# Kernel tuning notes

Measured on AMD Instinct MI355X. Metric: run time of the kernel, lower is better.

## Reference

```python
import jax, jax.numpy as jnp
import numpy as np

LOWRES = 256  # low-res input to coefficient tower
GB = 16       # spatial_bins (grid H=W)
LB = 8        # luma_bins (grid depth)
NIN, NOUT = 3, 3


def _conv_s2(x, w, b):
    # 3x3 stride-2 conv, torch padding=1
    y = jax.lax.conv_general_dilated(x, w, (2, 2), ((1, 1), (1, 1)),
                                     dimension_numbers=('NCHW', 'OIHW', 'NCHW'))
    return y + b[None, :, None, None]


def _pw(x, w, b):
    # 1x1 conv as einsum; w: [O, C]
    return jnp.einsum('bchw,oc->bohw', x, w) + b[None, :, None, None]


def _bilateral_slice(grid, guide, image):
    # grid [B,12,L,GH,GW]; guide [B,H,W] in [0,1]; image [B,NIN,H,W]
    B, C, L, GH, GW = grid.shape
    H, W = guide.shape[1], guide.shape[2]
    cx = (jnp.arange(W, dtype=jnp.float32) + 0.5) * (GW / W) - 0.5
    cy = (jnp.arange(H, dtype=jnp.float32) + 0.5) * (GH / H) - 0.5
    cz = guide * L - 0.5
    x0f = jnp.floor(cx); wx = cx - x0f
    y0f = jnp.floor(cy); wy = cy - y0f
    z0f = jnp.floor(cz); wz = cz - z0f
    x0 = x0f.astype(jnp.int32); y0 = y0f.astype(jnp.int32); z0 = z0f.astype(jnp.int32)
    bidx = jnp.arange(B)[:, None, None]
    acc = jnp.zeros((B, H, W, C), jnp.float32)
    for dz in (0, 1):
        zi = jnp.clip(z0 + dz, 0, L - 1)                     # [B,H,W]
        wzz = wz if dz else (1.0 - wz)
        for dy in (0, 1):
            yi = jnp.clip(y0 + dy, 0, GH - 1)[None, :, None]
            wyy = (wy if dy else (1.0 - wy))[None, :, None]
            for dx in (0, 1):
                xi = jnp.clip(x0 + dx, 0, GW - 1)[None, None, :]
                wxx = (wx if dx else (1.0 - wx))[None, None, :]
                g = grid[bidx, :, zi, yi, xi]                # [B,H,W,C]
                acc = acc + (wzz * wyy * wxx)[..., None] * g
    aff = acc.reshape(B, H, W, NOUT, NIN + 1)
    out = jnp.einsum('bhwci,bihw->bchw', aff[..., :NIN], image) \
        + jnp.transpose(aff[..., NIN], (0, 3, 1, 2))
    return out


def reference(image, val, sw0, sb0, sw1, sb1, sw2, sb2, sw3, sb3, spw, spb,
              lw1, lb1, lw2, lb2, lw3, lb3, cw, cb, fw1, fb1, fw2, fb2,
              gw, gb, ccm_w, ccm_b, shifts, slopes, prw, prb):
    B = image.shape[0]
    low = jax.image.resize(image, (B, NIN, LOWRES, LOWRES), 'bilinear', antialias=False)
    # splat tower: 4 stride-2 3x3 convs + final 1x1 (no relu)
    x = jax.nn.relu(_conv_s2(low, sw0, sb0))
    x = jax.nn.relu(_conv_s2(x, sw1, sb1))
    x = jax.nn.relu(_conv_s2(x, sw2, sb2))
    x = jax.nn.relu(_conv_s2(x, sw3, sb3))           # [B,64,16,16]
    splat = _pw(x, spw, spb) + val                   # + conditioning value
    # local path: three 1x1 convs with relu
    loc = jax.nn.relu(_pw(splat, lw1, lb1))
    loc = jax.nn.relu(_pw(loc, lw2, lb2))
    loc = jax.nn.relu(_pw(loc, lw3, lb3))            # [B,64,16,16]
    # condition path: 1x1 stride-2 conv -> adaptive avgpool(4) -> 2 fc layers
    c = jax.nn.relu(_pw(splat[:, :, ::2, ::2], cw, cb))  # [B,4,8,8]
    c = c.reshape(B, 4, 4, 2, 4, 2).mean(axis=(3, 5))    # [B,4,4,4]
    c = c.reshape(B, 64)
    c = jax.nn.relu(c @ fw1.T + fb1)
    c = jax.nn.relu(c @ fw2.T + fb2)                 # [B,64]
    fused = jax.nn.relu(c[:, :, None, None] + loc)
    coeff = _pw(fused, gw, gb)                       # [B,96,16,16]
    # split into LB chunks of 12 along channels, stack at dim 2
    grid = coeff.reshape(B, LB, NOUT * (NIN + 1), GB, GB).transpose(0, 2, 1, 3, 4)
    # guidemap: ccm -> piecewise-linear curve -> projection -> hardtanh [0,1]
    g = _pw(image, ccm_w, ccm_b)                     # [B,3,H,W]
    g = (slopes * jax.nn.relu(g[..., None] - shifts[None])).sum(-1)
    g = _pw(g, prw, prb)[:, 0]                       # [B,H,W]
    guide = jnp.clip(g, 0.0, 1.0)
    return _bilateral_slice(grid, guide, image)


def setup_inputs() -> dict:
    rng = np.random.default_rng(0)
    def rn(shape, fan_in):
        return jnp.asarray(rng.standard_normal(shape).astype(np.float32) * np.sqrt(2.0 / fan_in))
    B, H, W = 4, 1024, 1024
    d = {}
    d['image'] = jnp.asarray(rng.random((B, 3, H, W), dtype=np.float32))
    d['val'] = jnp.asarray(rng.random((B, 1, 1, 1), dtype=np.float32))
    # splat tower 3->8->16->32->64
    chans = [(3, 8), (8, 16), (16, 32), (32, 64)]
    for i, (ci, co) in enumerate(chans):
        d[f'sw{i}'] = rn((co, ci, 3, 3), ci * 9)
        d[f'sb{i}'] = jnp.zeros((co,), jnp.float32)
    d['spw'] = rn((64, 64), 64); d['spb'] = jnp.zeros((64,), jnp.float32)
    d['lw1'] = rn((128, 64), 64); d['lb1'] = jnp.zeros((128,), jnp.float32)
    d['lw2'] = rn((128, 128), 128); d['lb2'] = jnp.zeros((128,), jnp.float32)
    d['lw3'] = rn((64, 128), 128); d['lb3'] = jnp.zeros((64,), jnp.float32)
    d['cw'] = rn((4, 64), 64); d['cb'] = jnp.zeros((4,), jnp.float32)
    d['fw1'] = rn((64, 64), 64); d['fb1'] = jnp.zeros((64,), jnp.float32)
    d['fw2'] = rn((64, 64), 64); d['fb2'] = jnp.zeros((64,), jnp.float32)
    d['gw'] = rn((96, 64), 64); d['gb'] = jnp.zeros((96,), jnp.float32)
    # guide params (mirrors make_guide_params init)
    d['ccm_w'] = jnp.asarray(np.identity(3, dtype=np.float32)
                             + rng.standard_normal((3, 3)).astype(np.float32) * 1e-4)
    d['ccm_b'] = jnp.zeros((3,), jnp.float32)
    shifts = np.linspace(0, 1, 16, endpoint=False, dtype=np.float32)[None, None, None, :]
    d['shifts'] = jnp.asarray(np.tile(shifts, (3, 1, 1, 1)))
    slopes = np.zeros((1, 3, 1, 1, 16), dtype=np.float32); slopes[..., 0] = 1.0
    d['slopes'] = jnp.asarray(slopes)
    d['prw'] = jnp.ones((1, 3), jnp.float32) / 3.0
    d['prb'] = jnp.zeros((1,), jnp.float32)
    return d
```

## Files before the change

kernel.cpp:

```cpp
#include <hip/hip_runtime.h>

#define BATCH 4
#define HH 1024
#define WW 1024

__global__ __launch_bounds__(256) void ds01_k(const float* __restrict__ img,
                                              const float* __restrict__ w0,
                                              const float* __restrict__ b0,
                                              const float* __restrict__ w1,
                                              const float* __restrict__ b1,
                                              float* __restrict__ out) {
  int blk = blockIdx.x;
  int tx = blk & 15;
  int ty = (blk >> 4) & 15;
  int b = blk >> 8;
  int t = threadIdx.x;

  __shared__ float low[3][19][21];
  __shared__ float x0s[8][9][12];

  int Y0 = ty << 2, X0 = tx << 2;
  int gy0 = 2 * Y0 - 1, gx0 = 2 * X0 - 1;
  int ly0 = 2 * gy0 - 1, lx0 = 2 * gx0 - 1;

  for (int i = t; i < 3 * 19 * 19; i += 256) {
    int c = i / 361;
    int rem = i - c * 361;
    int ly = rem / 19;
    int lx = rem - ly * 19;
    int gy = ly0 + ly, gx = lx0 + lx;
    float v = 0.f;
    if (gy >= 0 && gx >= 0) {
      const float* p = img + (size_t)(b * 3 + c) * HH * WW + (4 * gy + 1) * WW + 4 * gx;
      float4 u0 = *(const float4*)p;
      float4 u1 = *(const float4*)(p + WW);
      v = 0.25f * (u0.y + u0.z + u1.y + u1.z);
    }
    low[c][ly][lx] = v;
  }
  __syncthreads();

  for (int i = t; i < 8 * 81; i += 256) {
    int ch = i / 81;
    int pos = i - ch * 81;
    int py = pos / 9, px = pos - py * 9;
    int gy = gy0 + py, gx = gx0 + px;
    float v = 0.f;
    if (gy >= 0 && gx >= 0) {
      float a = b0[ch];
#pragma unroll
      for (int ci = 0; ci < 3; ++ci)
#pragma unroll
        for (int ky = 0; ky < 3; ++ky)
#pragma unroll
          for (int kx = 0; kx < 3; ++kx)
            a += low[ci][2 * py + ky][2 * px + kx] *
                 w0[ch * 27 + ci * 9 + ky * 3 + kx];
      v = fmaxf(a, 0.f);
    }
    x0s[ch][py][px] = v;
  }
  __syncthreads();

  {
    int oc = t >> 4;
    int pos = t & 15;
    int y = pos >> 2, x = pos & 3;
    float a = b1[oc];
#pragma unroll
    for (int ci = 0; ci < 8; ++ci)
#pragma unroll
      for (int ky = 0; ky < 3; ++ky)
#pragma unroll
        for (int kx = 0; kx < 3; ++kx)
          a += x0s[ci][2 * y + ky][2 * x + kx] *
               w1[(oc * 8 + ci) * 9 + ky * 3 + kx];
    out[(size_t)(b * 16 + oc) * 64 * 64 + (Y0 + y) * 64 + X0 + x] =
        fmaxf(a, 0.f);
  }
}

template <int CI, int CO, int HI, int P>
__global__ __launch_bounds__(256) void conv_tile_k(const float* __restrict__ in,
                                                   const float* __restrict__ wgt,
                                                   const float* __restrict__ bias,
                                                   float* __restrict__ out) {
  const int HO = HI / 2;
  const int NT = HO / P;
  const int HALO = 2 * P + 1;
  const int RS = 2 * P + 4;
  constexpr int NO = (CO * P * P) / 256;
  int blk = blockIdx.x;
  int tx = blk % NT;
  int ty = (blk / NT) % NT;
  int b = blk / (NT * NT);
  int t = threadIdx.x;

  __shared__ float s[CI][HALO][RS];

  int Y0 = ty * P, X0 = tx * P;
  int gy0 = 2 * Y0 - 1, gx0 = 2 * X0 - 1;

  for (int i = t; i < CI * HALO * HALO; i += 256) {
    int c = i / (HALO * HALO);
    int rem = i - c * (HALO * HALO);
    int ly = rem / HALO;
    int lx = rem - ly * HALO;
    int gy = gy0 + ly, gx = gx0 + lx;
    float v = 0.f;
    if (gy >= 0 && gy < HI && gx >= 0 && gx < HI)
      v = in[((size_t)(b * CI + c) * HI + gy) * HI + gx];
    s[c][ly][lx] = v;
  }
  __syncthreads();

  int px = t % (P * P);
  int og = t / (P * P);
  int x = px % P, y = px / P;
  float acc[NO];
#pragma unroll
  for (int j = 0; j < NO; ++j) acc[j] = bias[og * NO + j];
  for (int ci = 0; ci < CI; ++ci) {
#pragma unroll
    for (int ky = 0; ky < 3; ++ky) {
#pragma unroll
      for (int kx = 0; kx < 3; ++kx) {
        float v = s[ci][2 * y + ky][2 * x + kx];
#pragma unroll
        for (int j = 0; j < NO; ++j)
          acc[j] += wgt[((og * NO + j) * CI + ci) * 9 + ky * 3 + kx] * v;
      }
    }
  }
#pragma unroll
  for (int j = 0; j < NO; ++j)
    out[(size_t)(b * CO + og * NO + j) * HO * HO + (Y0 + y) * HO + X0 + x] =
        fmaxf(acc[j], 0.f);
}

template <int CI, int RELU>
__device__ __forceinline__ void pw4_c64(const float (*__restrict__ X)[4],
                                        float (*__restrict__ Y)[4],
                                        const float* __restrict__ w,
                                        const float* __restrict__ bias,
                                        float badd, int t) {
  int u = t & 3, og = t >> 2;
  float acc = bias[og] + badd;
#pragma unroll 4
  for (int k = 0; k < CI; k += 4) {
    float4 wv = *(const float4*)&w[og * CI + k];
    acc += wv.x * X[k][u] + wv.y * X[k + 1][u] + wv.z * X[k + 2][u] +
           wv.w * X[k + 3][u];
  }
  if (RELU) acc = fmaxf(acc, 0.f);
  Y[og][u] = acc;
}

template <int CI, int RELU>
__device__ __forceinline__ void pw4_c128(const float (*__restrict__ X)[4],
                                         float (*__restrict__ Y)[4],
                                         const float* __restrict__ w,
                                         const float* __restrict__ bias,
                                         int t) {
  int u0 = (t & 1) << 1, og = t >> 1;
  float a0 = bias[og], a1 = a0;
#pragma unroll 4
  for (int k = 0; k < CI; k += 4) {
    float4 wv = *(const float4*)&w[og * CI + k];
    float2 x0 = *(const float2*)&X[k][u0];
    float2 x1 = *(const float2*)&X[k + 1][u0];
    float2 x2 = *(const float2*)&X[k + 2][u0];
    float2 x3v = *(const float2*)&X[k + 3][u0];
    a0 += wv.x * x0.x + wv.y * x1.x + wv.z * x2.x + wv.w * x3v.x;
    a1 += wv.x * x0.y + wv.y * x1.y + wv.z * x2.y + wv.w * x3v.y;
  }
  if (RELU) { a0 = fmaxf(a0, 0.f); a1 = fmaxf(a1, 0.f); }
  Y[og][u0] = a0;
  Y[og][u0 + 1] = a1;
}

__global__ __launch_bounds__(256) void mlp_k(
    const float* __restrict__ x3, const float* __restrict__ spw,
    const float* __restrict__ spb, const float* __restrict__ val,
    const float* __restrict__ lw1, const float* __restrict__ lb1,
    const float* __restrict__ lw2, const float* __restrict__ lb2,
    const float* __restrict__ lw3, const float* __restrict__ lb3,
    const float* __restrict__ cw, const float* __restrict__ cb,
    const float* __restrict__ fw1, const float* __restrict__ fb1,
    const float* __restrict__ fw2, const float* __restrict__ fb2,
    const float* __restrict__ gw, const float* __restrict__ gb,
    float* __restrict__ gridt) {
  int blk = blockIdx.x;
  int b = blk >> 6;
  int p0 = (blk & 63) << 2;
  int t = threadIdx.x;

  __shared__ __align__(16) float A[128][4];
  __shared__ __align__(16) float Bf[128][4];
  __shared__ float effs[4][64];
  __shared__ float ebv[4];
  __shared__ float s8v[4][64];
  __shared__ float scv[64], h1v[64], f2v[64];

  A[t >> 2][t & 3] = x3[((size_t)(b * 64 + (t >> 2))) * 256 + p0 + (t & 3)];
  {
    int ch = t >> 6, k = t & 63;
    float a = 0.f;
#pragma unroll 8
    for (int o = 0; o < 64; ++o) a += cw[ch * 64 + o] * spw[o * 64 + k];
    effs[ch][k] = a;
    if (k == 0) {
      float a2 = 0.f;
      float vb = val[b];
#pragma unroll 8
      for (int o = 0; o < 64; ++o) a2 += cw[ch * 64 + o] * (spb[o] + vb);
      ebv[ch] = cb[ch] + a2;
    }
  }
  __syncthreads();
  {
    int ch = t >> 6, i = t & 63;
    int p = ((i >> 3) << 5) + ((i & 7) << 1);
    float a = ebv[ch];
#pragma unroll 8
    for (int k = 0; k < 64; ++k)
      a += effs[ch][k] * x3[((size_t)(b * 64 + k)) * 256 + p];
    s8v[ch][i] = fmaxf(a, 0.f);
  }
  __syncthreads();
  if (t < 64) {
    int ch = t >> 4, q = t & 15;
    int py = q >> 2, qx = q & 3;
    int i0 = (py * 2) * 8 + qx * 2;
    scv[t] = 0.25f * (s8v[ch][i0] + s8v[ch][i0 + 1] + s8v[ch][i0 + 8] +
                      s8v[ch][i0 + 9]);
  }
  __syncthreads();

  if (t < 64) {
    float a = fb1[t];
#pragma unroll 8
    for (int k = 0; k < 64; ++k) a += fw1[t * 64 + k] * scv[k];
    h1v[t] = fmaxf(a, 0.f);
  }
  pw4_c64<64, 0>(A, Bf, spw, spb, val[b], t);
  __syncthreads();
  if (t < 64) {
    float a = fb2[t];
#pragma unroll 8
    for (int k = 0; k < 64; ++k) a += fw2[t * 64 + k] * h1v[k];
    f2v[t] = fmaxf(a, 0.f);
  }
  pw4_c128<64, 1>(Bf, A, lw1, lb1, t);
  __syncthreads();
  pw4_c128<128, 1>(A, Bf, lw2, lb2, t);
  __syncthreads();
  pw4_c64<128, 1>(Bf, A, lw3, lb3, 0.f, t);
  __syncthreads();

  {
    int u0 = (t & 1) << 1, og = t >> 1;
    if (og < 96) {
      float a0 = gb[og], a1 = a0;
#pragma unroll 4
      for (int k = 0; k < 64; k += 4) {
        float4 cc4 = *(const float4*)&f2v[k];
        float2 x0 = *(const float2*)&A[k][u0];
        float2 x1 = *(const float2*)&A[k + 1][u0];
        float2 x2 = *(const float2*)&A[k + 2][u0];
        float2 x3v = *(const float2*)&A[k + 3][u0];
        x0.x = fmaxf(x0.x + cc4.x, 0.f); x0.y = fmaxf(x0.y + cc4.x, 0.f);
        x1.x = fmaxf(x1.x + cc4.y, 0.f); x1.y = fmaxf(x1.y + cc4.y, 0.f);
        x2.x = fmaxf(x2.x + cc4.z, 0.f); x2.y = fmaxf(x2.y + cc4.z, 0.f);
        x3v.x = fmaxf(x3v.x + cc4.w, 0.f); x3v.y = fmaxf(x3v.y + cc4.w, 0.f);
        float4 wv = *(const float4*)&gw[og * 64 + k];
        a0 += wv.x * x0.x + wv.y * x1.x + wv.z * x2.x + wv.w * x3v.x;
        a1 += wv.x * x0.y + wv.y * x1.y + wv.z * x2.y + wv.w * x3v.y;
      }
      int l = og / 12, cc = og - l * 12;
      gridt[(size_t)(((b * 8 + l) << 8) + p0 + u0) * 12 + cc] = a0;
      gridt[(size_t)(((b * 8 + l) << 8) + p0 + u0 + 1) * 12 + cc] = a1;
    }
  }
}

#define ZST 200
__global__ __launch_bounds__(256, 6) void slice_k(
    const float* __restrict__ img, const float* __restrict__ gridt,
    const float* __restrict__ ccm_w, const float* __restrict__ ccm_b,
    const float* __restrict__ shifts, const float* __restrict__ slopes,
    const float* __restrict__ prw, const float* __restrict__ prb,
    float* __restrict__ out) {
  int blk = blockIdx.x;
  int b = blk >> 10;
  int h = blk & 1023;
  int t = threadIdx.x;

  __shared__ float sg[8 * ZST];
  __shared__ float2 lut[3][16];

  float cy = (h + 0.5f) * 0.015625f - 0.5f;
  float y0f = floorf(cy);
  float wy = cy - y0f;
  int y0 = (int)y0f;
  int yi0 = min(max(y0, 0), 15), yi1 = min(max(y0 + 1, 0), 15);

  if (t < 48) {
    int c = t >> 4, k = t & 15;
    float cs = 0.f, cbv = 0.f;
    for (int i = 0; i <= k; ++i) {
      float s = slopes[c * 16 + i];
      cs += s;
      cbv += s * shifts[c * 16 + i];
    }
    lut[c][k] = make_float2(cs, cbv);
  }

  for (int i = t; i < 384; i += 256) {
    int z = i / 48;
    int e = i - z * 48;
    const float4* s0 =
        (const float4*)(gridt + (size_t)(((b * 8 + z) << 8) + (yi0 << 4)) * 12);
    const float4* s1 =
        (const float4*)(gridt + (size_t)(((b * 8 + z) << 8) + (yi1 << 4)) * 12);
    float4 a = s0[e], c = s1[e];
    float4 v = make_float4(a.x + wy * (c.x - a.x), a.y + wy * (c.y - a.y),
                           a.z + wy * (c.z - a.z), a.w + wy * (c.w - a.w));
    *((float4*)(sg + z * ZST) + e) = v;
  }
  __syncthreads();

  int pp = (h << 10) + (t << 2);
  const float* ib = img + (size_t)b * 3 * HH * WW;
  float4 R4 = *(const float4*)(ib + pp);
  float4 G4 = *(const float4*)(ib + HH * WW + pp);
  float4 B4 = *(const float4*)(ib + 2 * HH * WW + pp);
  float r_[4] = {R4.x, R4.y, R4.z, R4.w};
  float g_[4] = {G4.x, G4.y, G4.z, G4.w};
  float b_[4] = {B4.x, B4.y, B4.z, B4.w};

  float m0 = ccm_w[0], m1 = ccm_w[1], m2 = ccm_w[2];
  float m3 = ccm_w[3], m4 = ccm_w[4], m5 = ccm_w[5];
  float m6 = ccm_w[6], m7 = ccm_w[7], m8 = ccm_w[8];
  float c0 = ccm_b[0], c1 = ccm_b[1], c2 = ccm_b[2];
  float p0 = prw[0], p1 = prw[1], p2 = prw[2], pb = prb[0];

  float base0 = shifts[0], base1 = shifts[16], base2 = shifts[32];
  float inv0 = 1.0f / (shifts[1] - base0);
  float inv1 = 1.0f / (shifts[17] - base1);
  float inv2 = 1.0f / (shifts[33] - base2);

  float ro[4], go[4], bo[4];
#pragma unroll
  for (int j = 0; j < 4; ++j) {
    float r = r_[j], g = g_[j], bl = b_[j];
    float v0 = c0 + m0 * r + m1 * g + m2 * bl;
    float v1 = c1 + m3 * r + m4 * g + m5 * bl;
    float v2 = c2 + m6 * r + m7 * g + m8 * bl;

    float tv0 = fmaxf(v0, base0);
    float tv1 = fmaxf(v1, base1);
    float tv2 = fmaxf(v2, base2);
    int j0 = min((int)((tv0 - base0) * inv0), 15);
    int j1 = min((int)((tv1 - base1) * inv1), 15);
    int j2 = min((int)((tv2 - base2) * inv2), 15);
    float2 e0 = lut[0][j0];
    float2 e1 = lut[1][j1];
    float2 e2 = lut[2][j2];
    float f0 = e0.x * tv0 - e0.y;
    float f1 = e1.x * tv1 - e1.y;
    float f2 = e2.x * tv2 - e2.y;

    float gg = pb + p0 * f0 + p1 * f1 + p2 * f2;
    float guide = fminf(fmaxf(gg, 0.f), 1.f);

    int w = (t << 2) + j;
    float cx = (w + 0.5f) * 0.015625f - 0.5f;
    float x0f = floorf(cx);
    float wx = cx - x0f;
    int x0i = (int)x0f;
    int xi0 = min(max(x0i, 0), 15), xi1 = min(max(x0i + 1, 0), 15);

    float cz = guide * 8.0f - 0.5f;
    float z0f = floorf(cz);
    float wz = cz - z0f;
    int z0i = (int)z0f;
    int zi0 = min(max(z0i, 0), 7), zi1 = min(max(z0i + 1, 0), 7);

    int oz0 = zi0 * ZST, oz1 = zi1 * ZST;
    int ox0 = xi0 * 12, ox1 = xi1 * 12;
    float wz1 = wz, wz0 = 1.f - wz;
    float wx1 = wx, wx0 = 1.f - wx;

    float rr = 0.f, gg2 = 0.f, bb2 = 0.f;
#pragma unroll
    for (int dz = 0; dz < 2; ++dz) {
      int oz = dz ? oz1 : oz0;
      float wzz = dz ? wz1 : wz0;
#pragma unroll
      for (int dx = 0; dx < 2; ++dx) {
        int ox = dx ? ox1 : ox0;
        float wgt = wzz * (dx ? wx1 : wx0);
        const float* gp = sg + oz + ox;
        float4 a0 = *(const float4*)gp;
        float4 a1 = *(const float4*)(gp + 4);
        float4 a2 = *(const float4*)(gp + 8);
        rr  += wgt * (a0.x * r + a0.y * g + a0.z * bl + a0.w);
        gg2 += wgt * (a1.x * r + a1.y * g + a1.z * bl + a1.w);
        bb2 += wgt * (a2.x * r + a2.y * g + a2.z * bl + a2.w);
      }
    }
    ro[j] = rr;
    go[j] = gg2;
    bo[j] = bb2;
  }
  float* ob = out + (size_t)b * 3 * HH * WW;
  *(float4*)(ob + pp) = make_float4(ro[0], ro[1], ro[2], ro[3]);
  *(float4*)(ob + HH * WW + pp) = make_float4(go[0], go[1], go[2], go[3]);
  *(float4*)(ob + 2 * HH * WW + pp) = make_float4(bo[0], bo[1], bo[2], bo[3]);
}

extern "C" void kernel_launch(void* const* d_in, const int* in_sizes, int n_in,
                              void* d_out, int out_size, void* d_ws, size_t ws_size,
                              hipStream_t stream) {
  const float* image = (const float*)d_in[0];
  const float* val   = (const float*)d_in[1];
  const float* sw0 = (const float*)d_in[2];  const float* sb0 = (const float*)d_in[3];
  const float* sw1 = (const float*)d_in[4];  const float* sb1 = (const float*)d_in[5];
  const float* sw2 = (const float*)d_in[6];  const float* sb2 = (const float*)d_in[7];
  const float* sw3 = (const float*)d_in[8];  const float* sb3 = (const float*)d_in[9];
  const float* spw = (const float*)d_in[10]; const float* spb = (const float*)d_in[11];
  const float* lw1 = (const float*)d_in[12]; const float* lb1 = (const float*)d_in[13];
  const float* lw2 = (const float*)d_in[14]; const float* lb2 = (const float*)d_in[15];
  const float* lw3 = (const float*)d_in[16]; const float* lb3 = (const float*)d_in[17];
  const float* cw  = (const float*)d_in[18]; const float* cb  = (const float*)d_in[19];
  const float* fw1 = (const float*)d_in[20]; const float* fb1 = (const float*)d_in[21];
  const float* fw2 = (const float*)d_in[22]; const float* fb2 = (const float*)d_in[23];
  const float* gw  = (const float*)d_in[24]; const float* gb  = (const float*)d_in[25];
  const float* ccm_w = (const float*)d_in[26]; const float* ccm_b = (const float*)d_in[27];
  const float* shifts = (const float*)d_in[28]; const float* slopes = (const float*)d_in[29];
  const float* prw = (const float*)d_in[30]; const float* prb = (const float*)d_in[31];
  float* out = (float*)d_out;

  float* ws    = (float*)d_ws;
  float* x0    = ws;
  float* x1    = x0 + 524288;
  float* x2    = x1 + 262144;
  float* x3    = x2 + 131072;
  float* gridt = x3 + 65536 + 256;

  ds01_k<<<1024, 256, 0, stream>>>(image, sw0, sb0, sw1, sb1, x1);
  conv_tile_k<16, 32, 64, 4><<<256, 256, 0, stream>>>(x1, sw2, sb2, x2);
  conv_tile_k<32, 64, 32, 2><<<256, 256, 0, stream>>>(x2, sw3, sb3, x3);
  mlp_k<<<256, 256, 0, stream>>>(x3, spw, spb, val, lw1, lb1, lw2, lb2, lw3, lb3,
                                 cw, cb, fw1, fb1, fw2, fb2, gw, gb, gridt);
  slice_k<<<4096, 256, 0, stream>>>(image, gridt, ccm_w, ccm_b, shifts, slopes,
                                    prw, prb, out);
}
```

Measured before the change: 223.1 us.

## Fuse conv2, conv3 and MLP into one persistent kernel with grid barriers

Merges the two strided conv kernels and the MLP/grid kernel into a single 256-block kernel that separates stages with atomic-counter grid barriers. The counters are reset inside ds01_k. The aim is to remove two kernel launch gaps on tiny stages. The risks are barrier spin cost, and a deadlock if all 256 blocks are not co-resident, though the MI355X has enough CUs for this.

```diff
diff --git a/kernel.cpp b/kernel.cpp
--- a/kernel.cpp
+++ b/kernel.cpp
@@ -3,18 +3,32 @@
 #define BATCH 4
 #define HH 1024
 #define WW 1024
+
+__device__ __forceinline__ void gbar(unsigned* cnt) {
+  __syncthreads();
+  __threadfence();
+  if (threadIdx.x == 0) {
+    atomicAdd(cnt, 1u);
+    while (atomicAdd(cnt, 0u) < 256u) __builtin_amdgcn_s_sleep(2);
+  }
+  __syncthreads();
+  __threadfence();
+}
 
 __global__ __launch_bounds__(256) void ds01_k(const float* __restrict__ img,
                                               const float* __restrict__ w0,
                                               const float* __restrict__ b0,
                                               const float* __restrict__ w1,
                                               const float* __restrict__ b1,
-                                              float* __restrict__ out) {
+                                              float* __restrict__ out,
+                                              unsigned* __restrict__ cnt) {
   int blk = blockIdx.x;
   int tx = blk & 15;
   int ty = (blk >> 4) & 15;
   int b = blk >> 8;
   int t = threadIdx.x;
+
+  if (blk == 0 && t < 2) cnt[t] = 0;
 
   __shared__ float low[3][19][21];
   __shared__ float x0s[8][9][12];
@@ -80,108 +94,14 @@
   }
 }
 
-template <int CI, int CO, int HI, int P>
-__global__ __launch_bounds__(256) void conv_tile_k(const float* __restrict__ in,
-                                                   const float* __restrict__ wgt,
-                                                   const float* __restrict__ bias,
-                                                   float* __restrict__ out) {
-  const int HO = HI / 2;
-  const int NT = HO / P;
-  const int HALO = 2 * P + 1;
-  const int RS = 2 * P + 4;
-  constexpr int NO = (CO * P * P) / 256;
-  int blk = blockIdx.x;
-  int tx = blk % NT;
-  int ty = (blk / NT) % NT;
-  int b = blk / (NT * NT);
-  int t = threadIdx.x;
-
-  __shared__ float s[CI][HALO][RS];
-
-  int Y0 = ty * P, X0 = tx * P;
-  int gy0 = 2 * Y0 - 1, gx0 = 2 * X0 - 1;
-
-  for (int i = t; i < CI * HALO * HALO; i += 256) {
-    int c = i / (HALO * HALO);
-    int rem = i - c * (HALO * HALO);
-    int ly = rem / HALO;
-    int lx = rem - ly * HALO;
-    int gy = gy0 + ly, gx = gx0 + lx;
-    float v = 0.f;
-    if (gy >= 0 && gy < HI && gx >= 0 && gx < HI)
-      v = in[((size_t)(b * CI + c) * HI + gy) * HI + gx];
-    s[c][ly][lx] = v;
-  }
-  __syncthreads();
-
-  int px = t % (P * P);
-  int og = t / (P * P);
-  int x = px % P, y = px / P;
-  float acc[NO];
-#pragma unroll
-  for (int j = 0; j < NO; ++j) acc[j] = bias[og * NO + j];
-  for (int ci = 0; ci < CI; ++ci) {
-#pragma unroll
-    for (int ky = 0; ky < 3; ++ky) {
-#pragma unroll
-      for (int kx = 0; kx < 3; ++kx) {
-        float v = s[ci][2 * y + ky][2 * x + kx];
-#pragma unroll
-        for (int j = 0; j < NO; ++j)
-          acc[j] += wgt[((og * NO + j) * CI + ci) * 9 + ky * 3 + kx] * v;
-      }
-    }
-  }
-#pragma unroll
-  for (int j = 0; j < NO; ++j)
-    out[(size_t)(b * CO + og * NO + j) * HO * HO + (Y0 + y) * HO + X0 + x] =
-        fmaxf(acc[j], 0.f);
-}
-
-template <int CI, int RELU>
-__device__ __forceinline__ void pw4_c64(const float (*__restrict__ X)[4],
-                                        float (*__restrict__ Y)[4],
-                                        const float* __restrict__ w,
-                                        const float* __restrict__ bias,
-                                        float badd, int t) {
-  int u = t & 3, og = t >> 2;
-  float acc = bias[og] + badd;
-#pragma unroll 4
-  for (int k = 0; k < CI; k += 4) {
-    float4 wv = *(const float4*)&w[og * CI + k];
-    acc += wv.x * X[k][u] + wv.y * X[k + 1][u] + wv.z * X[k + 2][u] +
-           wv.w * X[k + 3][u];
-  }
-  if (RELU) acc = fmaxf(acc, 0.f);
-  Y[og][u] = acc;
-}
-
-template <int CI, int RELU>
-__device__ __forceinline__ void pw4_c128(const float (*__restrict__ X)[4],
-                                         float (*__restrict__ Y)[4],
-                                         const float* __restrict__ w,
-                                         const float* __restrict__ bias,
-                                         int t) {
-  int u0 = (t & 1) << 1, og = t >> 1;
-  float a0 = bias[og], a1 = a0;
-#pragma unroll 4
-  for (int k = 0; k < CI; k += 4) {
-    float4 wv = *(const float4*)&w[og * CI + k];
-    float2 x0 = *(const float2*)&X[k][u0];
-    float2 x1 = *(const float2*)&X[k + 1][u0];
-    float2 x2 = *(const float2*)&X[k + 2][u0];
-    float2 x3v = *(const float2*)&X[k + 3][u0];
-    a0 += wv.x * x0.x + wv.y * x1.x + wv.z * x2.x + wv.w * x3v.x;
-    a1 += wv.x * x0.y + wv.y * x1.y + wv.z * x2.y + wv.w * x3v.y;
-  }
-  if (RELU) { a0 = fmaxf(a0, 0.f); a1 = fmaxf(a1, 0.f); }
-  Y[og][u0] = a0;
-  Y[og][u0 + 1] = a1;
-}
-
-__global__ __launch_bounds__(256) void mlp_k(
-    const float* __restrict__ x3, const float* __restrict__ spw,
-    const float* __restrict__ spb, const float* __restrict__ val,
+__global__ __launch_bounds__(256, 1) void mid_k(
+    const float* __restrict__ x1,
+    const float* __restrict__ sw2, const float* __restrict__ sb2,
+    float* __restrict__ x2,
+    const float* __restrict__ sw3, const float* __restrict__ sb3,
+    float* __restrict__ x3,
+    const float* __restrict__ spw, const float* __restrict__ spb,
+    const float* __restrict__ val,
     const float* __restrict__ lw1, const float* __restrict__ lb1,
     const float* __restrict__ lw2, const float* __restrict__ lb2,
     const float* __restrict__ lw3, const float* __restrict__ lb3,
@@ -189,12 +109,12 @@
     const float* __restrict__ fw1, const float* __restrict__ fb1,
     const float* __restrict__ fw2, const float* __restrict__ fb2,
     const float* __restrict__ gw, const float* __restrict__ gb,
-    float* __restrict__ gridt) {
+    float* __restrict__ gridt, unsigned* __restrict__ cnt) {
   int blk = blockIdx.x;
-  int b = blk >> 6;
-  int p0 = (blk & 63) << 2;
   int t = threadIdx.x;
 
+  __shared__ float s2[16][9][12];
+  __shared__ float s3[32][5][8];
   __shared__ __align__(16) float A[128][4];
   __shared__ __align__(16) float Bf[128][4];
   __shared__ float effs[4][64];
@@ -202,84 +122,201 @@
   __shared__ float s8v[4][64];
   __shared__ float scv[64], h1v[64], f2v[64];
 
-  A[t >> 2][t & 3] = x3[((size_t)(b * 64 + (t >> 2))) * 256 + p0 + (t & 3)];
   {
-    int ch = t >> 6, k = t & 63;
-    float a = 0.f;
+    int tx = blk & 7, ty = (blk >> 3) & 7, b = blk >> 6;
+    int Y0 = ty * 4, X0 = tx * 4;
+    int gy0 = 2 * Y0 - 1, gx0 = 2 * X0 - 1;
+    for (int i = t; i < 16 * 81; i += 256) {
+      int c = i / 81;
+      int rem = i - c * 81;
+      int ly = rem / 9, lx = rem - ly * 9;
+      int gy = gy0 + ly, gx = gx0 + lx;
+      float v = 0.f;
+      if (gy >= 0 && gy < 64 && gx >= 0 && gx < 64)
+        v = x1[((size_t)(b * 16 + c) * 64 + gy) * 64 + gx];
+      s2[c][ly][lx] = v;
+    }
+    __syncthreads();
+    int px = t & 15, og = t >> 4;
+    int x = px & 3, y = px >> 2;
+    float a0 = sb2[og * 2], a1 = sb2[og * 2 + 1];
+    for (int ci = 0; ci < 16; ++ci) {
+#pragma unroll
+      for (int ky = 0; ky < 3; ++ky)
+#pragma unroll
+        for (int kx = 0; kx < 3; ++kx) {
+          float v = s2[ci][2 * y + ky][2 * x + kx];
+          a0 += sw2[((og * 2) * 16 + ci) * 9 + ky * 3 + kx] * v;
+          a1 += sw2[((og * 2 + 1) * 16 + ci) * 9 + ky * 3 + kx] * v;
+        }
+    }
+    x2[(size_t)(b * 32 + og * 2) * 1024 + (Y0 + y) * 32 + X0 + x] = fmaxf(a0, 0.f);
+    x2[(size_t)(b * 32 + og * 2 + 1) * 1024 + (Y0 + y) * 32 + X0 + x] = fmaxf(a1, 0.f);
+  }
+  gbar(cnt + 0);
+
+  {
+    int tx = blk & 7, ty = (blk >> 3) & 7, b = blk >> 6;
+    int Y0 = ty * 2, X0 = tx * 2;
+    int gy0 = 2 * Y0 - 1, gx0 = 2 * X0 - 1;
+    for (int i = t; i < 32 * 25; i += 256) {
+      int c = i / 25;
+      int rem = i - c * 25;
+      int ly = rem / 5, lx = rem - ly * 5;
+      int gy = gy0 + ly, gx = gx0 + lx;
+      float v = 0.f;
+      if (gy >= 0 && gy < 32 && gx >= 0 && gx < 32)
+        v = x2[((size_t)(b * 32 + c) * 32 + gy) * 32 + gx];
+      s3[c][ly][lx] = v;
+    }
+    __syncthreads();
+    int px = t & 3, og = t >> 2;
+    int x = px & 1, y = px >> 1;
+    float a = sb3[og];
+    for (int ci = 0; ci < 32; ++ci) {
+#pragma unroll
+      for (int ky = 0; ky < 3; ++ky)
+#pragma unroll
+        for (int kx = 0; kx < 3; ++kx)
+          a += sw3[(og * 32 + ci) * 9 + ky * 3 + kx] *
+               s3[ci][2 * y + ky][2 * x + kx];
+    }
+    x3[(size_t)(b * 64 + og) * 256 + (Y0 + y) * 16 + X0 + x] = fmaxf(a, 0.f);
+  }
+  gbar(cnt + 1);
+
+  {
+    int b = blk >> 6;
+    int p0 = (blk & 63) << 2;
+
+    A[t >> 2][t & 3] = x3[((size_t)(b * 64 + (t >> 2))) * 256 + p0 + (t & 3)];
+    {
+      int ch = t >> 6, k = t & 63;
+      float a = 0.f;
 #pragma unroll 8
-    for (int o = 0; o < 64; ++o) a += cw[ch * 64 + o] * spw[o * 64 + k];
-    effs[ch][k] = a;
-    if (k == 0) {
-      float a2 = 0.f;
-      float vb = val[b];
+      for (int o = 0; o < 64; ++o) a += cw[ch * 64 + o] * spw[o * 64 + k];
+      effs[ch][k] = a;
+      if (k == 0) {
+        float a2 = 0.f;
+        float vb = val[b];
 #pragma unroll 8
-      for (int o = 0; o < 64; ++o) a2 += cw[ch * 64 + o] * (spb[o] + vb);
-      ebv[ch] = cb[ch] + a2;
-    }
-  }
-  __syncthreads();
-  {
-    int ch = t >> 6, i = t & 63;
-    int p = ((i >> 3) << 5) + ((i & 7) << 1);
-    float a = ebv[ch];
+        for (int o = 0; o < 64; ++o) a2 += cw[ch * 64 + o] * (spb[o] + vb);
+        ebv[ch] = cb[ch] + a2;
+      }
+    }
+    __syncthreads();
+    {
+      int ch = t >> 6, i = t & 63;
+      int p = ((i >> 3) << 5) + ((i & 7) << 1);
+      float a = ebv[ch];
 #pragma unroll 8
-    for (int k = 0; k < 64; ++k)
-      a += effs[ch][k] * x3[((size_t)(b * 64 + k)) * 256 + p];
-    s8v[ch][i] = fmaxf(a, 0.f);
-  }
-  __syncthreads();
-  if (t < 64) {
-    int ch = t >> 4, q = t & 15;
-    int py = q >> 2, qx = q & 3;
-    int i0 = (py * 2) * 8 + qx * 2;
-    scv[t] = 0.25f * (s8v[ch][i0] + s8v[ch][i0 + 1] + s8v[ch][i0 + 8] +
-                      s8v[ch][i0 + 9]);
-  }
-  __syncthreads();
-
-  if (t < 64) {
-    float a = fb1[t];
+      for (int k = 0; k < 64; ++k)
+        a += effs[ch][k] * x3[((size_t)(b * 64 + k)) * 256 + p];
+      s8v[ch][i] = fmaxf(a, 0.f);
+    }
+    __syncthreads();
+    if (t < 64) {
+      int ch = t >> 4, q = t & 15;
+      int py = q >> 2, qx = q & 3;
+      int i0 = (py * 2) * 8 + qx * 2;
+      scv[t] = 0.25f * (s8v[ch][i0] + s8v[ch][i0 + 1] + s8v[ch][i0 + 8] +
+                        s8v[ch][i0 + 9]);
+    }
+    __syncthreads();
+
+    if (t < 64) {
+      float a = fb1[t];
 #pragma unroll 8
-    for (int k = 0; k < 64; ++k) a += fw1[t * 64 + k] * scv[k];
-    h1v[t] = fmaxf(a, 0.f);
-  }
-  pw4_c64<64, 0>(A, Bf, spw, spb, val[b], t);
-  __syncthreads();
-  if (t < 64) {
-    float a = fb2[t];
-#pragma unroll 8
-    for (int k = 0; k < 64; ++k) a += fw2[t * 64 + k] * h1v[k];
-    f2v[t] = fmaxf(a, 0.f);
-  }
-  pw4_c128<64, 1>(Bf, A, lw1, lb1, t);
-  __syncthreads();
-  pw4_c128<128, 1>(A, Bf, lw2, lb2, t);
-  __syncthreads();
-  pw4_c64<128, 1>(Bf, A, lw3, lb3, 0.f, t);
-  __syncthreads();
-
-  {
-    int u0 = (t & 1) << 1, og = t >> 1;
-    if (og < 96) {
-      float a0 = gb[og], a1 = a0;
+      for (int k = 0; k < 64; ++k) a += fw1[t * 64 + k] * scv[k];
+      h1v[t] = fmaxf(a, 0.f);
+    }
+    {
+      int u = t & 3, og = t >> 2;
+      float acc = spb[og] + val[b];
 #pragma unroll 4
       for (int k = 0; k < 64; k += 4) {
-        float4 cc4 = *(const float4*)&f2v[k];
-        float2 x0 = *(const float2*)&A[k][u0];
-        float2 x1 = *(const float2*)&A[k + 1][u0];
-        float2 x2 = *(const float2*)&A[k + 2][u0];
-        float2 x3v = *(const float2*)&A[k + 3][u0];
-        x0.x = fmaxf(x0.x + cc4.x, 0.f); x0.y = fmaxf(x0.y + cc4.x, 0.f);
-        x1.x = fmaxf(x1.x + cc4.y, 0.f); x1.y = fmaxf(x1.y + cc4.y, 0.f);
-        x2.x = fmaxf(x2.x + cc4.z, 0.f); x2.y = fmaxf(x2.y + cc4.z, 0.f);
-        x3v.x = fmaxf(x3v.x + cc4.w, 0.f); x3v.y = fmaxf(x3v.y + cc4.w, 0.f);
-        float4 wv = *(const float4*)&gw[og * 64 + k];
-        a0 += wv.x * x0.x + wv.y * x1.x + wv.z * x2.x + wv.w * x3v.x;
-        a1 += wv.x * x0.y + wv.y * x1.y + wv.z * x2.y + wv.w * x3v.y;
-      }
-      int l = og / 12, cc = og - l * 12;
-      gridt[(size_t)(((b * 8 + l) << 8) + p0 + u0) * 12 + cc] = a0;
-      gridt[(size_t)(((b * 8 + l) << 8) + p0 + u0 + 1) * 12 + cc] = a1;
+        float4 wv = *(const float4*)&spw[og * 64 + k];
+        acc += wv.x * A[k][u] + wv.y * A[k + 1][u] + wv.z * A[k + 2][u] +
+               wv.w * A[k + 3][u];
+      }
+      Bf[og][u] = acc;
+    }
+    __syncthreads();
+    if (t < 64) {
+      float a = fb2[t];
+#pragma unroll 8
+      for (int k = 0; k < 64; ++k) a += fw2[t * 64 + k] * h1v[k];
+      f2v[t] = fmaxf(a, 0.f);
+    }
+    {
+      int u0 = (t & 1) << 1, og = t >> 1;
+      float a0 = lb1[og], a1 = a0;
+#pragma unroll 4
+      for (int k = 0; k < 64; k += 4) {
+        float4 wv = *(const float4*)&lw1[og * 64 + k];
+        float2 q0 = *(const float2*)&Bf[k][u0];
+        float2 q1 = *(const float2*)&Bf[k + 1][u0];
+        float2 q2 = *(const float2*)&Bf[k + 2][u0];
+        float2 q3 = *(const float2*)&Bf[k + 3][u0];
+        a0 += wv.x * q0.x + wv.y * q1.x + wv.z * q2.x + wv.w * q3.x;
+        a1 += wv.x * q0.y + wv.y * q1.y + wv.z * q2.y + wv.w * q3.y;
+      }
+      A[og][u0] = fmaxf(a0, 0.f);
+      A[og][u0 + 1] = fmaxf(a1, 0.f);
+    }
+    __syncthreads();
+    {
+      int u0 = (t & 1) << 1, og = t >> 1;
+      float a0 = lb2[og], a1 = a0;
+#pragma unroll 4
+      for (int k = 0; k < 128; k += 4) {
+        float4 wv = *(const float4*)&lw2[og * 128 + k];
+        float2 q0 = *(const float2*)&A[k][u0];
+        float2 q1 = *(const float2*)&A[k + 1][u0];
+        float2 q2 = *(const float2*)&A[k + 2][u0];
+        float2 q3 = *(const float2*)&A[k + 3][u0];
+        a0 += wv.x * q0.x + wv.y * q1.x + wv.z * q2.x + wv.w * q3.x;
+        a1 += wv.x * q0.y + wv.y * q1.y + wv.z * q2.y + wv.w * q3.y;
+      }
+      Bf[og][u0] = fmaxf(a0, 0.f);
+      Bf[og][u0 + 1] = fmaxf(a1, 0.f);
+    }
+    __syncthreads();
+    {
+      int u = t & 3, og = t >> 2;
+      float acc = lb3[og];
+#pragma unroll 4
+      for (int k = 0; k < 128; k += 4) {
+        float4 wv = *(const float4*)&lw3[og * 128 + k];
+        acc += wv.x * Bf[k][u] + wv.y * Bf[k + 1][u] + wv.z * Bf[k + 2][u] +
+               wv.w * Bf[k + 3][u];
+      }
+      A[og][u] = fmaxf(acc, 0.f);
+    }
+    __syncthreads();
+    {
+      int u0 = (t & 1) << 1, og = t >> 1;
+      if (og < 96) {
+        float a0 = gb[og], a1 = a0;
+#pragma unroll 4
+        for (int k = 0; k < 64; k += 4) {
+          float4 cc4 = *(const float4*)&f2v[k];
+          float2 q0 = *(const float2*)&A[k][u0];
+          float2 q1 = *(const float2*)&A[k + 1][u0];
+          float2 q2 = *(const float2*)&A[k + 2][u0];
+          float2 q3 = *(const float2*)&A[k + 3][u0];
+          q0.x = fmaxf(q0.x + cc4.x, 0.f); q0.y = fmaxf(q0.y + cc4.x, 0.f);
+          q1.x = fmaxf(q1.x + cc4.y, 0.f); q1.y = fmaxf(q1.y + cc4.y, 0.f);
+          q2.x = fmaxf(q2.x + cc4.z, 0.f); q2.y = fmaxf(q2.y + cc4.z, 0.f);
+          q3.x = fmaxf(q3.x + cc4.w, 0.f); q3.y = fmaxf(q3.y + cc4.w, 0.f);
+          float4 wv = *(const float4*)&gw[og * 64 + k];
+          a0 += wv.x * q0.x + wv.y * q1.x + wv.z * q2.x + wv.w * q3.x;
+          a1 += wv.x * q0.y + wv.y * q1.y + wv.z * q2.y + wv.w * q3.y;
+        }
+        int l = og / 12, cc = og - l * 12;
+        gridt[(size_t)(((b * 8 + l) << 8) + p0 + u0) * 12 + cc] = a0;
+        gridt[(size_t)(((b * 8 + l) << 8) + p0 + u0 + 1) * 12 + cc] = a1;
+      }
     }
   }
 }
@@ -448,12 +485,12 @@
   float* x2    = x1 + 262144;
   float* x3    = x2 + 131072;
   float* gridt = x3 + 65536 + 256;
-
-  ds01_k<<<1024, 256, 0, stream>>>(image, sw0, sb0, sw1, sb1, x1);
-  conv_tile_k<16, 32, 64, 4><<<256, 256, 0, stream>>>(x1, sw2, sb2, x2);
-  conv_tile_k<32, 64, 32, 2><<<256, 256, 0, stream>>>(x2, sw3, sb3, x3);
-  mlp_k<<<256, 256, 0, stream>>>(x3, spw, spb, val, lw1, lb1, lw2, lb2, lw3, lb3,
-                                 cw, cb, fw1, fb1, fw2, fb2, gw, gb, gridt);
+  unsigned* cnt = (unsigned*)(gridt + 98304);
+
+  ds01_k<<<1024, 256, 0, stream>>>(image, sw0, sb0, sw1, sb1, x1, cnt);
+  mid_k<<<256, 256, 0, stream>>>(x1, sw2, sb2, x2, sw3, sb3, x3,
+                                 spw, spb, val, lw1, lb1, lw2, lb2, lw3, lb3,
+                                 cw, cb, fw1, fb1, fw2, fb2, gw, gb, gridt, cnt);
   slice_k<<<4096, 256, 0, stream>>>(image, gridt, ccm_w, ccm_b, shifts, slopes,
                                     prw, prb, out);
 }
```

Result: slower. 301.9 us (+35.3%).
